# Kernel tuning notes

Hardware: AMD Instinct MI355X
Metric: run time of the kernel (lower is better)

The kernel has to match this reference:

```python
import jax, jax.numpy as jnp
import numpy as np

B, S, D = 4, 4096, 64

def setup_inputs() -> dict:
    key = jax.random.key(0)
    ks = jax.random.split(key, 6)
    mk = lambda k: jax.random.normal(k, (B, S, D), dtype=jnp.float32)
    return {
        "q_re": mk(ks[0]), "q_im": mk(ks[1]),
        "k_re": mk(ks[2]), "k_im": mk(ks[3]),
        "v_re": mk(ks[4]), "v_im": mk(ks[5]),
    }

def reference(q_re, q_im, k_re, k_im, v_re, v_im):
    # Complex QK^T (no conjugate, matching torch.bmm on complex tensors):
    # (qr + i qi)(kr + i ki)^T -> re = qr kr^T - qi ki^T ; im = qr ki^T + qi kr^T
    d_k = q_re.shape[-1]
    scale = 1.0 / jnp.sqrt(jnp.asarray(d_k, dtype=q_re.dtype))
    s_re = (jnp.einsum('bqd,bkd->bqk', q_re, k_re)
            - jnp.einsum('bqd,bkd->bqk', q_im, k_im)) * scale
    s_im = (jnp.einsum('bqd,bkd->bqk', q_re, k_im)
            + jnp.einsum('bqd,bkd->bqk', q_im, k_re)) * scale
    # softmax over |scores| along key axis; weights are real (imag part is 0)
    w = jax.nn.softmax(jnp.sqrt(s_re * s_re + s_im * s_im), axis=-1)  # [B,S,S]
    # CVDropout is identity in eval mode. Output = real_weights @ complex_values
    o_re = jnp.einsum('bqk,bkd->bqd', w, v_re)
    o_im = jnp.einsum('bqk,bkd->bqd', w, v_im)
    return jnp.stack([o_re, o_im], axis=0)  # [2, B, S, D] (real, imag)
```

## Files before the change

### kernel.cpp

```cpp
#include <hip/hip_runtime.h>
#include <stdint.h>

#define B_    4
#define S_    4096
#define D_    64
#define QBLK  64
#define NELEM (B_ * S_ * D_)
#define BS_   (B_ * S_)

typedef __attribute__((ext_vector_type(8))) short bf16x8;
typedef __attribute__((ext_vector_type(4))) short bf16x4;
typedef __attribute__((ext_vector_type(4))) float f32x4;
typedef __attribute__((ext_vector_type(4))) int   i32x4;
typedef __attribute__((ext_vector_type(4))) unsigned u32x4;
typedef __attribute__((ext_vector_type(4))) _Float16 f16x4;

#define MFMA(a, b, c) __builtin_amdgcn_mfma_f32_16x16x32_bf16(a, b, c, 0, 0, 0)
#define VMWAIT(n) asm volatile("s_waitcnt vmcnt(" #n ")" ::: "memory")
#define BARRIER() do { asm volatile("" ::: "memory"); __builtin_amdgcn_s_barrier(); asm volatile("" ::: "memory"); } while (0)
#define LGKM_FENCE() do { asm volatile("s_waitcnt lgkmcnt(0)" ::: "memory"); __builtin_amdgcn_sched_barrier(0); } while (0)

__device__ __forceinline__ short f2bf(float x) {
    unsigned u = __builtin_bit_cast(unsigned, x);
    u += 0x7FFFu + ((u >> 16) & 1u);
    return (short)(u >> 16);
}

__device__ __forceinline__ unsigned cvtpk(float lo, float hi) {
    unsigned r;
    asm("v_cvt_pk_bf16_f32 %0, %1, %2" : "=v"(r) : "v"(lo), "v"(hi));
    return r;
}

__device__ __forceinline__ void async16(const short* g, short* l) {
    __builtin_amdgcn_global_load_lds(
        (const __attribute__((address_space(1))) unsigned int*)g,
        (__attribute__((address_space(3))) unsigned int*)l, 16, 0, 0);
}

__global__ __launch_bounds__(256)
void prepass_kernel(const float* __restrict__ q_re, const float* __restrict__ q_im,
                    const float* __restrict__ k_re, const float* __restrict__ k_im,
                    const float* __restrict__ v_re, const float* __restrict__ v_im,
                    short* __restrict__ ws) {
    const int bidx = blockIdx.x;
    const int tid  = threadIdx.x;
    if (bidx < 4096) {
        const int idx = bidx * 256 + tid;
        const int tn  = idx >> 18;
        const int e4  = idx & ((1 << 18) - 1);
        const float* s = (tn == 0 ? q_re : tn == 1 ? q_im : tn == 2 ? k_re : k_im)
                         + (size_t)e4 * 4;
        const float sc = (tn < 2) ? 0.125f : 1.0f;
        f32x4 x = *(const f32x4*)s;
        bf16x4 v;
#pragma unroll
        for (int c = 0; c < 4; ++c) v[c] = f2bf(x[c] * sc);
        *(bf16x4*)(ws + (size_t)tn * NELEM + (size_t)e4 * 4) = v;
    } else {
        __shared__ short tile[64][72];
        const int tb   = bidx - 4096;
        const int sb   = tb & 63;
        const int b    = (tb >> 6) & 3;
        const int comp = tb >> 8;
        const float* src = comp ? v_im : v_re;
        short* dst = ws + (size_t)(4 + comp) * NELEM;
#pragma unroll
        for (int i = 0; i < 4; ++i) {
            const int slot = i * 256 + tid;
            const int s  = slot >> 4;
            const int d4 = slot & 15;
            f32x4 x = *(const f32x4*)(src + (((size_t)b * S_) + sb * 64 + s) * D_ + d4 * 4);
#pragma unroll
            for (int c = 0; c < 4; ++c) tile[d4 * 4 + c][s] = f2bf(x[c]);
        }
        __syncthreads();
#pragma unroll
        for (int i = 0; i < 2; ++i) {
            const int slot = i * 256 + tid;
            const int d = slot >> 3;
            const int m = slot & 7;
            const int a = m >> 2, hh = m & 3;
            bf16x8 v;
#pragma unroll
            for (int j = 0; j < 8; ++j)
                v[j] = tile[d][a * 32 + hh * 4 + ((j >> 2) << 4) + (j & 3)];
            *(bf16x8*)(dst + ((size_t)b * 64 + d) * S_ + sb * 64 + m * 8) = v;
        }
    }
}

template<int SPLIT, typename OT>
__global__ __launch_bounds__(256, 4)
void cv_attn_main(const short* __restrict__ wsb,
                  float* __restrict__ out,
                  OT* __restrict__ opart,
                  float* __restrict__ ml)
{
    __shared__ __align__(16) short smem[2 * 8192];

    const int tid  = threadIdx.x;
    const int lane = tid & 63;
    const int wv   = tid >> 6;
    const int l15  = lane & 15;
    const int h    = lane >> 4;

    int bid = blockIdx.x;
    const int nwg = B_ * 64 * SPLIT;
    bid = (bid & 7) * (nwg >> 3) + (bid >> 3);
    const int qb = bid & 63;
    const int sp = (bid >> 6) % SPLIT;
    const int b  = bid / (64 * SPLIT);

    const short* qr = wsb;
    const short* qi = wsb + (size_t)NELEM;
    const short* kr = wsb + 2 * (size_t)NELEM;
    const short* ki = wsb + 3 * (size_t)NELEM;
    const short* vT = wsb + 4 * (size_t)NELEM;

    const short* p0 = smem + l15 * 64 + ((h ^ (l15 & 7)) << 3);
    const short* p1 = smem + l15 * 64 + (((h ^ 4) ^ (l15 & 7)) << 3);

    const int qrow = qb * QBLK + wv * 16 + l15;
    const size_t qoff = ((size_t)b * S_ + qrow) * D_;
    bf16x8 fqr[2], fqi[2];
#pragma unroll
    for (int dh = 0; dh < 2; ++dh) {
        fqr[dh] = *(const bf16x8*)(qr + qoff + dh * 32 + h * 8);
        fqi[dh] = *(const bf16x8*)(qi + qoff + dh * 32 + h * 8);
    }

    f32x4 o_re[4], o_im[4];
#pragma unroll
    for (int i = 0; i < 4; ++i) {
        o_re[i] = (f32x4){0.f, 0.f, 0.f, 0.f};
        o_im[i] = (f32x4){0.f, 0.f, 0.f, 0.f};
    }
    float m_run = -1e30f, l_run = 0.f;
    const float L2E = 1.44269504088896f;

    const int srcg = (lane & 7) ^ (lane >> 3);
    const int kRow = wv * 8 + (lane >> 3);
    constexpr int TPB = (S_ / 32) / SPLIT;

    auto stageK = [&](int t, int DST) {
        const int kb = (sp * TPB + t) * 32;
        const size_t koff = ((size_t)b * S_ + kb + kRow) * 64 + (srcg << 3);
        async16(kr + koff, smem + DST + wv * 512);
        async16(ki + koff, smem + DST + 2048 + wv * 512);
    };
    auto stageV = [&](int t, int DST) {
        const int kb = (sp * TPB + t) * 32;
#pragma unroll
        for (int i = 0; i < 2; ++i) {
            const int d = (wv + 4 * i) * 8 + (lane >> 3);
            const short* src = vT + ((srcg >> 2) ? (size_t)NELEM : (size_t)0)
                               + ((size_t)b * 64 + d) * S_ + kb + (srcg & 3) * 8;
            async16(src, smem + DST + 4096 + wv * 512 + i * 2048);
        }
    };

    auto qk = [&](int CUR, f32x4 (&sre)[2], f32x4 (&sim)[2]) {
#pragma unroll
        for (int c = 0; c < 2; ++c) {
            sre[c] = (f32x4){0.f, 0.f, 0.f, 0.f};
            sim[c] = (f32x4){0.f, 0.f, 0.f, 0.f};
        }
        i32x4 n0 = __builtin_bit_cast(i32x4, fqi[0]) ^ (int)0x80008000;
        i32x4 n1 = __builtin_bit_cast(i32x4, fqi[1]) ^ (int)0x80008000;
        bf16x8 fn0 = __builtin_bit_cast(bf16x8, n0);
        bf16x8 fn1 = __builtin_bit_cast(bf16x8, n1);
        __builtin_amdgcn_s_setprio(1);
#pragma unroll
        for (int c = 0; c < 2; ++c) {
            bf16x8 a0 = *(const bf16x8*)(p0 + CUR + c * 1024);
            bf16x8 a1 = *(const bf16x8*)(p1 + CUR + c * 1024);
            bf16x8 b0 = *(const bf16x8*)(p0 + CUR + 2048 + c * 1024);
            bf16x8 b1 = *(const bf16x8*)(p1 + CUR + 2048 + c * 1024);
            sre[c] = MFMA(a0, fqr[0], sre[c]);
            sre[c] = MFMA(a1, fqr[1], sre[c]);
            sre[c] = MFMA(b0, fn0,    sre[c]);
            sre[c] = MFMA(b1, fn1,    sre[c]);
            sim[c] = MFMA(b0, fqr[0], sim[c]);
            sim[c] = MFMA(b1, fqr[1], sim[c]);
            sim[c] = MFMA(a0, fqi[0], sim[c]);
            sim[c] = MFMA(a1, fqi[1], sim[c]);
        }
        __builtin_amdgcn_s_setprio(0);
    };

    auto spv = [&](int CUR, f32x4 (&sre)[2], f32x4 (&sim)[2]) {
#pragma unroll
        for (int c = 0; c < 2; ++c) {
            f32x4 g = sre[c] * sre[c] + sim[c] * sim[c];
#pragma unroll
            for (int r = 0; r < 4; ++r) sre[c][r] = __builtin_amdgcn_sqrtf(g[r]);
        }
        float tmax = fmaxf(fmaxf(fmaxf(sre[0][0], sre[0][1]), fmaxf(sre[0][2], sre[0][3])),
                           fmaxf(fmaxf(sre[1][0], sre[1][1]), fmaxf(sre[1][2], sre[1][3])));
        tmax = fmaxf(tmax, __shfl_xor(tmax, 16));
        tmax = fmaxf(tmax, __shfl_xor(tmax, 32));
        if (__any(tmax > m_run + 8.0f)) {
            const float m_new = fmaxf(m_run, tmax);
            const float alpha = __builtin_amdgcn_exp2f((m_run - m_new) * L2E);
            l_run *= alpha;
#pragma unroll
            for (int i = 0; i < 4; ++i) { o_re[i] *= alpha; o_im[i] *= alpha; }
            m_run = m_new;
        }
        const float nm = -m_run * L2E;
#pragma unroll
        for (int c = 0; c < 2; ++c)
#pragma unroll
            for (int r = 0; r < 4; ++r)
                sim[c][r] = __builtin_amdgcn_exp2f(__builtin_fmaf(sre[c][r], L2E, nm));
        f32x4 ps = sim[0] + sim[1];
        l_run += (ps[0] + ps[1]) + (ps[2] + ps[3]);

        u32x4 w;
        w[0] = cvtpk(sim[0][0], sim[0][1]);
        w[1] = cvtpk(sim[0][2], sim[0][3]);
        w[2] = cvtpk(sim[1][0], sim[1][1]);
        w[3] = cvtpk(sim[1][2], sim[1][3]);
        bf16x8 pb = __builtin_bit_cast(bf16x8, w);

        __builtin_amdgcn_s_setprio(1);
#pragma unroll
        for (int dc = 0; dc < 4; ++dc) {
            bf16x8 av = *(const bf16x8*)(p0 + CUR + 4096 + dc * 1024);
            bf16x8 ai = *(const bf16x8*)(p1 + CUR + 4096 + dc * 1024);
            o_re[dc] = MFMA(av, pb, o_re[dc]);
            o_im[dc] = MFMA(ai, pb, o_im[dc]);
        }
        __builtin_amdgcn_s_setprio(0);
    };

    auto body = [&](int t, int CUR, int NXT,
                    f32x4 (&cre)[2], f32x4 (&cim)[2],
                    f32x4 (&nre)[2], f32x4 (&nim)[2]) {
        VMWAIT(0);
        LGKM_FENCE();
        BARRIER();
        if (t + 2 < TPB) stageK(t + 2, CUR);
        if (t + 1 < TPB) {
            stageV(t + 1, NXT);
            qk(NXT, nre, nim);
        }
        spv(CUR, cre, cim);
    };

    f32x4 sAre[2], sAim[2], sBre[2], sBim[2];
    stageK(0, 0);
    stageV(0, 0);
    stageK(1, 8192);
    VMWAIT(0);
    BARRIER();
    qk(0, sAre, sAim);

    for (int t = 0; t < TPB; t += 2) {
        body(t,     0,    8192, sAre, sAim, sBre, sBim);
        body(t + 1, 8192, 0,    sBre, sBim, sAre, sAim);
    }

    float lt = l_run;
    lt += __shfl_xor(lt, 16);
    lt += __shfl_xor(lt, 32);
    const float inv = 1.0f / lt;

    float* ol = (float*)smem;

    OT* dst_re;
    OT* dst_im;
    if constexpr (SPLIT == 1) {
        dst_re = (OT*)out + ((size_t)b * S_ + qb * QBLK) * D_;
        dst_im = dst_re + (size_t)NELEM;
    } else {
        const size_t qo = ((size_t)b * S_ + qb * QBLK) * D_;
        dst_re = opart + ((size_t)sp * 2 + 0) * NELEM + qo;
        dst_im = opart + ((size_t)sp * 2 + 1) * NELEM + qo;
    }

    auto store_comp = [&](const f32x4 (&oc)[4], OT* og) {
        __syncthreads();
#pragma unroll
        for (int dc = 0; dc < 4; ++dc)
#pragma unroll
            for (int r = 0; r < 4; ++r)
                ol[(wv * 16 + l15) * 65 + dc * 16 + h * 4 + r] = oc[dc][r] * inv;
        __syncthreads();
#pragma unroll
        for (int i = 0; i < 4; ++i) {
            const int slot = i * 256 + tid;
            const int row  = slot >> 4;
            const int c4   = slot & 15;
            f32x4 v;
#pragma unroll
            for (int j = 0; j < 4; ++j) v[j] = ol[row * 65 + c4 * 4 + j];
            if constexpr (sizeof(OT) == 4) {
                *(f32x4*)((float*)og + (size_t)row * D_ + c4 * 4) = v;
            } else {
                f16x4 hv;
#pragma unroll
                for (int j = 0; j < 4; ++j) hv[j] = (_Float16)v[j];
                *(f16x4*)((_Float16*)og + (size_t)row * D_ + c4 * 4) = hv;
            }
        }
    };
    store_comp(o_re, dst_re);
    store_comp(o_im, dst_im);

    if constexpr (SPLIT > 1) {
        if (lane < 16) {
            const int row = qb * QBLK + wv * 16 + lane;
            const size_t mo = ((size_t)sp * BS_ + (size_t)b * S_ + row) * 2;
            ml[mo]     = m_run;
            ml[mo + 1] = lt;
        }
    }
}

template<int SPLIT, typename OT>
__global__ __launch_bounds__(256)
void cv_attn_combine(const OT* __restrict__ opart, const float* __restrict__ ml,
                     float* __restrict__ out) {
    const int idx  = blockIdx.x * 256 + threadIdx.x;
    const int d4   = idx & 15;
    const int rest = idx >> 4;
    const int row  = rest & (BS_ - 1);
    const int comp = rest >> 14;
    float ms[SPLIT], ls[SPLIT];
    float M = -1e30f;
#pragma unroll
    for (int s = 0; s < SPLIT; ++s) {
        ms[s] = ml[((size_t)s * BS_ + row) * 2];
        ls[s] = ml[((size_t)s * BS_ + row) * 2 + 1];
        M = fmaxf(M, ms[s]);
    }
    float W = 0.f;
    f32x4 acc = (f32x4){0.f, 0.f, 0.f, 0.f};
#pragma unroll
    for (int s = 0; s < SPLIT; ++s) {
        const float w = ls[s] * __builtin_amdgcn_exp2f((ms[s] - M) * 1.44269504088896f);
        W += w;
        const OT* op = opart + ((size_t)(s * 2 + comp)) * NELEM + (size_t)row * D_ + d4 * 4;
        f32x4 o;
        if constexpr (sizeof(OT) == 4) {
            o = *(const f32x4*)op;
        } else {
            f16x4 hv = *(const f16x4*)op;
#pragma unroll
            for (int j = 0; j < 4; ++j) o[j] = (float)hv[j];
        }
        acc += o * w;
    }
    acc *= (1.0f / W);
    *(f32x4*)(out + (size_t)comp * NELEM + (size_t)row * D_ + d4 * 4) = acc;
}

__global__ __launch_bounds__(256, 1)
void cv_attn_legacy(const float* __restrict__ q_re, const float* __restrict__ q_im,
                    const float* __restrict__ k_re, const float* __restrict__ k_im,
                    const float* __restrict__ v_re, const float* __restrict__ v_im,
                    float* __restrict__ out)
{
    __shared__ __align__(16) short smem[4 * 64 * D_];
    short* kr_s = smem;
    short* ki_s = smem + 4096;
    short* vr_s = smem + 8192;
    short* vi_s = smem + 12288;

    const int tid  = threadIdx.x;
    const int lane = tid & 63;
    const int wv   = tid >> 6;
    const int l15  = lane & 15;
    const int h    = lane >> 4;

    const int b  = blockIdx.x >> 6;
    const int qb = blockIdx.x & 63;
    const size_t boff = (size_t)b * S_ * D_;

    const int qrow = qb * QBLK + wv * 16 + l15;
    const float* qrp = q_re + boff + (size_t)qrow * D_;
    const float* qip = q_im + boff + (size_t)qrow * D_;
    bf16x8 fqr[2], fqi[2], fqn[2];
#pragma unroll
    for (int dh = 0; dh < 2; ++dh) {
        const int d0 = dh * 32 + h * 8;
        f32x4 a0 = *(const f32x4*)(qrp + d0);
        f32x4 a1 = *(const f32x4*)(qrp + d0 + 4);
        f32x4 b0 = *(const f32x4*)(qip + d0);
        f32x4 b1 = *(const f32x4*)(qip + d0 + 4);
#pragma unroll
        for (int j = 0; j < 4; ++j) {
            fqr[dh][j] = f2bf(a0[j]); fqr[dh][j + 4] = f2bf(a1[j]);
            fqi[dh][j] = f2bf(b0[j]); fqi[dh][j + 4] = f2bf(b1[j]);
            fqn[dh][j] = f2bf(-b0[j]); fqn[dh][j + 4] = f2bf(-b1[j]);
        }
    }

    f32x4 o_re[4], o_im[4];
#pragma unroll
    for (int i = 0; i < 4; ++i) {
        o_re[i] = (f32x4){0.f, 0.f, 0.f, 0.f};
        o_im[i] = (f32x4){0.f, 0.f, 0.f, 0.f};
    }
    float m_run = -1e30f, l_run = 0.f;
    const float SC = 0.125f * 1.44269504088896f;

    for (int t = 0; t < S_ / 64; ++t) {
        const int kb = t * 64;
#pragma unroll
        for (int a = 0; a < 2; ++a) {
            const float* src = (a ? k_im : k_re) + boff;
            short* dst = a ? ki_s : kr_s;
#pragma unroll
            for (int i = 0; i < 2; ++i) {
                const int slot = i * 256 + tid;
                const int row  = slot >> 3;
                const int cb   = slot & 7;
                const float* p = src + (size_t)(kb + row) * D_ + cb * 8;
                f32x4 x0 = *(const f32x4*)p;
                f32x4 x1 = *(const f32x4*)(p + 4);
                bf16x8 v;
#pragma unroll
                for (int j = 0; j < 4; ++j) { v[j] = f2bf(x0[j]); v[j + 4] = f2bf(x1[j]); }
                *(bf16x8*)(dst + row * 64 + ((cb ^ (row & 7)) << 3)) = v;
            }
        }
#pragma unroll
        for (int a = 0; a < 2; ++a) {
            const float* src = (a ? v_im : v_re) + boff;
            short* dst = a ? vi_s : vr_s;
#pragma unroll
            for (int i = 0; i < 4; ++i) {
                const int slot = i * 256 + tid;
                const int k  = slot >> 4;
                const int d4 = slot & 15;
                f32x4 x = *(const f32x4*)(src + (size_t)(kb + k) * D_ + d4 * 4);
#pragma unroll
                for (int c = 0; c < 4; ++c) {
                    const int d = d4 * 4 + c;
                    dst[d * 64 + (((k >> 2) ^ (d & 15)) << 2) + (k & 3)] = f2bf(x[c]);
                }
            }
        }
        __syncthreads();

        f32x4 s_re[4], s_im[4];
#pragma unroll
        for (int c = 0; c < 4; ++c) {
            s_re[c] = (f32x4){0.f, 0.f, 0.f, 0.f};
            s_im[c] = (f32x4){0.f, 0.f, 0.f, 0.f};
        }
#pragma unroll
        for (int c = 0; c < 4; ++c) {
            const int krow = c * 16 + l15;
#pragma unroll
            for (int dh = 0; dh < 2; ++dh) {
                const int u = ((dh * 4 + h) ^ (krow & 7)) << 3;
                bf16x8 fkr = *(const bf16x8*)(kr_s + krow * 64 + u);
                bf16x8 fki = *(const bf16x8*)(ki_s + krow * 64 + u);
                s_re[c] = MFMA(fkr, fqr[dh], s_re[c]);
                s_re[c] = MFMA(fki, fqn[dh], s_re[c]);
                s_im[c] = MFMA(fki, fqr[dh], s_im[c]);
                s_im[c] = MFMA(fkr, fqi[dh], s_im[c]);
            }
        }

        float pv[4][4];
        float tmax = 0.f;
#pragma unroll
        for (int c = 0; c < 4; ++c)
#pragma unroll
            for (int r = 0; r < 4; ++r) {
                const float re = s_re[c][r], im = s_im[c][r];
                const float mg = __builtin_amdgcn_sqrtf(re * re + im * im) * SC;
                pv[c][r] = mg;
                tmax = fmaxf(tmax, mg);
            }
        tmax = fmaxf(tmax, __shfl_xor(tmax, 16));
        tmax = fmaxf(tmax, __shfl_xor(tmax, 32));
        const float m_new = fmaxf(m_run, tmax);
        const float alpha = __builtin_amdgcn_exp2f(m_run - m_new);
        m_run = m_new;
        float psum = 0.f;
#pragma unroll
        for (int c = 0; c < 4; ++c)
#pragma unroll
            for (int r = 0; r < 4; ++r) {
                const float e = __builtin_amdgcn_exp2f(pv[c][r] - m_new);
                pv[c][r] = e;
                psum += e;
            }
        l_run = l_run * alpha + psum;
#pragma unroll
        for (int i = 0; i < 4; ++i) { o_re[i] *= alpha; o_im[i] *= alpha; }

        bf16x8 pb[2];
#pragma unroll
        for (int hf = 0; hf < 2; ++hf)
#pragma unroll
            for (int j = 0; j < 4; ++j) {
                pb[hf][j]     = f2bf(pv[hf * 2][j]);
                pb[hf][j + 4] = f2bf(pv[hf * 2 + 1][j]);
            }

#pragma unroll
        for (int hf = 0; hf < 2; ++hf) {
#pragma unroll
            for (int dc = 0; dc < 4; ++dc) {
                const int d  = dc * 16 + l15;
                const int s0 = (((hf * 8) + h)     ^ l15) << 2;
                const int s1 = (((hf * 8) + 4 + h) ^ l15) << 2;
                bf16x4 r0 = *(const bf16x4*)(vr_s + d * 64 + s0);
                bf16x4 r1 = *(const bf16x4*)(vr_s + d * 64 + s1);
                bf16x4 i0 = *(const bf16x4*)(vi_s + d * 64 + s0);
                bf16x4 i1 = *(const bf16x4*)(vi_s + d * 64 + s1);
                bf16x8 av, ai;
#pragma unroll
                for (int j = 0; j < 4; ++j) {
                    av[j] = r0[j]; av[j + 4] = r1[j];
                    ai[j] = i0[j]; ai[j + 4] = i1[j];
                }
                o_re[dc] = MFMA(av, pb[hf], o_re[dc]);
                o_im[dc] = MFMA(ai, pb[hf], o_im[dc]);
            }
        }
        __syncthreads();
    }

    float lt = l_run;
    lt += __shfl_xor(lt, 16);
    lt += __shfl_xor(lt, 32);
    const float inv = 1.0f / lt;

    float* ol = (float*)smem;
    auto store_comp = [&](const f32x4 (&oc)[4], float* og) {
#pragma unroll
        for (int dc = 0; dc < 4; ++dc)
#pragma unroll
            for (int r = 0; r < 4; ++r)
                ol[(wv * 16 + l15) * 65 + dc * 16 + h * 4 + r] = oc[dc][r] * inv;
        __syncthreads();
#pragma unroll
        for (int i = 0; i < 4; ++i) {
            const int slot = i * 256 + tid;
            const int row  = slot >> 4;
            const int c4   = slot & 15;
            f32x4 v;
#pragma unroll
            for (int j = 0; j < 4; ++j) v[j] = ol[row * 65 + c4 * 4 + j];
            *(f32x4*)(og + (size_t)row * D_ + c4 * 4) = v;
        }
        __syncthreads();
    };

    float* og0 = out + boff + (size_t)(qb * QBLK) * D_;
    store_comp(o_re, og0);
    store_comp(o_im, og0 + (size_t)B_ * S_ * D_);
}

extern "C" void kernel_launch(void* const* d_in, const int* in_sizes, int n_in,
                              void* d_out, int out_size, void* d_ws, size_t ws_size,
                              hipStream_t stream) {
    (void)in_sizes; (void)n_in; (void)out_size;
    const float* q_re = (const float*)d_in[0];
    const float* q_im = (const float*)d_in[1];
    const float* k_re = (const float*)d_in[2];
    const float* k_im = (const float*)d_in[3];
    const float* v_re = (const float*)d_in[4];
    const float* v_im = (const float*)d_in[5];
    float* out = (float*)d_out;

    const size_t bf_bytes = 6 * (size_t)NELEM * 2;
    const size_t need8f16 = bf_bytes + 8 * 2 * (size_t)NELEM * 2 + 8 * (size_t)BS_ * 8;
    const size_t need4f16 = bf_bytes + 4 * 2 * (size_t)NELEM * 2 + 4 * (size_t)BS_ * 8;

    if (ws_size >= bf_bytes) {
        short* wsb = (short*)d_ws;
        prepass_kernel<<<4608, 256, 0, stream>>>(q_re, q_im, k_re, k_im, v_re, v_im, wsb);
        char* extra = (char*)d_ws + bf_bytes;
        if (ws_size >= need8f16) {
            _Float16* opart = (_Float16*)extra;
            float* ml = (float*)(extra + 8 * 2 * (size_t)NELEM * 2);
            cv_attn_main<8, _Float16><<<B_ * 64 * 8, 256, 0, stream>>>(wsb, nullptr, opart, ml);
            cv_attn_combine<8, _Float16><<<2048, 256, 0, stream>>>(opart, ml, out);
        } else if (ws_size >= need4f16) {
            _Float16* opart = (_Float16*)extra;
            float* ml = (float*)(extra + 4 * 2 * (size_t)NELEM * 2);
            cv_attn_main<4, _Float16><<<B_ * 64 * 4, 256, 0, stream>>>(wsb, nullptr, opart, ml);
            cv_attn_combine<4, _Float16><<<2048, 256, 0, stream>>>(opart, ml, out);
        } else {
            cv_attn_main<1, float><<<B_ * 64, 256, 0, stream>>>(wsb, out, out, nullptr);
        }
    } else {
        cv_attn_legacy<<<B_ * 64, 256, 0, stream>>>(q_re, q_im, k_re, k_im, v_re, v_im, out);
    }
}
```

Measured before the change: 91.45 us.

## Double query block per workgroup to 128 rows with 512 threads, simplify pipeline

The main attention kernel now processes 128 query rows per workgroup with 8 waves, so each staged K/V tile in shared memory is reused by twice as many waves, which halves the global-to-LDS traffic per query. The previous software pipeline, which overlapped the QK product of the next tile with the softmax-PV of the current one, is replaced by a simpler double-buffered loop that stages the next tile and then runs QK and PV on the current tile. The output store is split into two halves to fit the existing LDS scratch. Dropping the QK lookahead may expose more latency per wave, and the larger blocks cut the number of workgroups in half.

Measured after the change: 81.40 us. 11.0% less time.

```diff
diff --git a/kernel.cpp b/kernel.cpp
--- a/kernel.cpp
+++ b/kernel.cpp
@@ -4,7 +4,7 @@
 #define B_    4
 #define S_    4096
 #define D_    64
-#define QBLK  64
+#define QBLK  128
 #define NELEM (B_ * S_ * D_)
 #define BS_   (B_ * S_)
 
@@ -91,7 +91,7 @@
 }
 
 template<int SPLIT, typename OT>
-__global__ __launch_bounds__(256, 4)
+__global__ __launch_bounds__(512, 4)
 void cv_attn_main(const short* __restrict__ wsb,
                   float* __restrict__ out,
                   OT* __restrict__ opart,
@@ -106,11 +106,11 @@
     const int h    = lane >> 4;
 
     int bid = blockIdx.x;
-    const int nwg = B_ * 64 * SPLIT;
+    const int nwg = B_ * 32 * SPLIT;
     bid = (bid & 7) * (nwg >> 3) + (bid >> 3);
-    const int qb = bid & 63;
-    const int sp = (bid >> 6) % SPLIT;
-    const int b  = bid / (64 * SPLIT);
+    const int qb = bid & 31;
+    const int sp = (bid >> 5) % SPLIT;
+    const int b  = bid / (32 * SPLIT);
 
     const short* qr = wsb;
     const short* qi = wsb + (size_t)NELEM;
@@ -140,31 +140,37 @@
     const float L2E = 1.44269504088896f;
 
     const int srcg = (lane & 7) ^ (lane >> 3);
-    const int kRow = wv * 8 + (lane >> 3);
     constexpr int TPB = (S_ / 32) / SPLIT;
 
-    auto stageK = [&](int t, int DST) {
+    auto stage = [&](int t, int DST) {
         const int kb = (sp * TPB + t) * 32;
-        const size_t koff = ((size_t)b * S_ + kb + kRow) * 64 + (srcg << 3);
-        async16(kr + koff, smem + DST + wv * 512);
-        async16(ki + koff, smem + DST + 2048 + wv * 512);
-    };
-    auto stageV = [&](int t, int DST) {
-        const int kb = (sp * TPB + t) * 32;
-#pragma unroll
-        for (int i = 0; i < 2; ++i) {
-            const int d = (wv + 4 * i) * 8 + (lane >> 3);
+        {
+            const int arr = wv >> 2;
+            const int w4  = wv & 3;
+            const int row = w4 * 8 + (lane >> 3);
+            const short* src = (arr ? ki : kr)
+                               + ((size_t)b * S_ + kb + row) * 64 + (srcg << 3);
+            async16(src, smem + DST + arr * 2048 + w4 * 512);
+        }
+        {
+            const int d = wv * 8 + (lane >> 3);
             const short* src = vT + ((srcg >> 2) ? (size_t)NELEM : (size_t)0)
                                + ((size_t)b * 64 + d) * S_ + kb + (srcg & 3) * 8;
-            async16(src, smem + DST + 4096 + wv * 512 + i * 2048);
+            async16(src, smem + DST + 4096 + wv * 512);
         }
     };
 
-    auto qk = [&](int CUR, f32x4 (&sre)[2], f32x4 (&sim)[2]) {
+    auto body = [&](int t, int CUR, int OTH) {
+        VMWAIT(0);
+        LGKM_FENCE();
+        BARRIER();
+        if (t + 1 < TPB) stage(t + 1, OTH);
+
+        f32x4 s_re[2], s_im[2];
 #pragma unroll
         for (int c = 0; c < 2; ++c) {
-            sre[c] = (f32x4){0.f, 0.f, 0.f, 0.f};
-            sim[c] = (f32x4){0.f, 0.f, 0.f, 0.f};
+            s_re[c] = (f32x4){0.f, 0.f, 0.f, 0.f};
+            s_im[c] = (f32x4){0.f, 0.f, 0.f, 0.f};
         }
         i32x4 n0 = __builtin_bit_cast(i32x4, fqi[0]) ^ (int)0x80008000;
         i32x4 n1 = __builtin_bit_cast(i32x4, fqi[1]) ^ (int)0x80008000;
@@ -177,29 +183,28 @@
             bf16x8 a1 = *(const bf16x8*)(p1 + CUR + c * 1024);
             bf16x8 b0 = *(const bf16x8*)(p0 + CUR + 2048 + c * 1024);
             bf16x8 b1 = *(const bf16x8*)(p1 + CUR + 2048 + c * 1024);
-            sre[c] = MFMA(a0, fqr[0], sre[c]);
-            sre[c] = MFMA(a1, fqr[1], sre[c]);
-            sre[c] = MFMA(b0, fn0,    sre[c]);
-            sre[c] = MFMA(b1, fn1,    sre[c]);
-            sim[c] = MFMA(b0, fqr[0], sim[c]);
-            sim[c] = MFMA(b1, fqr[1], sim[c]);
-            sim[c] = MFMA(a0, fqi[0], sim[c]);
-            sim[c] = MFMA(a1, fqi[1], sim[c]);
+            s_re[c] = MFMA(a0, fqr[0], s_re[c]);
+            s_re[c] = MFMA(a1, fqr[1], s_re[c]);
+            s_re[c] = MFMA(b0, fn0,    s_re[c]);
+            s_re[c] = MFMA(b1, fn1,    s_re[c]);
+            s_im[c] = MFMA(b0, fqr[0], s_im[c]);
+            s_im[c] = MFMA(b1, fqr[1], s_im[c]);
+            s_im[c] = MFMA(a0, fqi[0], s_im[c]);
+            s_im[c] = MFMA(a1, fqi[1], s_im[c]);
         }
         __builtin_amdgcn_s_setprio(0);
-    };
-
-    auto spv = [&](int CUR, f32x4 (&sre)[2], f32x4 (&sim)[2]) {
+
 #pragma unroll
         for (int c = 0; c < 2; ++c) {
-            f32x4 g = sre[c] * sre[c] + sim[c] * sim[c];
-#pragma unroll
-            for (int r = 0; r < 4; ++r) sre[c][r] = __builtin_amdgcn_sqrtf(g[r]);
-        }
-        float tmax = fmaxf(fmaxf(fmaxf(sre[0][0], sre[0][1]), fmaxf(sre[0][2], sre[0][3])),
-                           fmaxf(fmaxf(sre[1][0], sre[1][1]), fmaxf(sre[1][2], sre[1][3])));
+            f32x4 g = s_re[c] * s_re[c] + s_im[c] * s_im[c];
+#pragma unroll
+            for (int r = 0; r < 4; ++r) s_re[c][r] = __builtin_amdgcn_sqrtf(g[r]);
+        }
+        float tmax = fmaxf(fmaxf(fmaxf(s_re[0][0], s_re[0][1]), fmaxf(s_re[0][2], s_re[0][3])),
+                           fmaxf(fmaxf(s_re[1][0], s_re[1][1]), fmaxf(s_re[1][2], s_re[1][3])));
         tmax = fmaxf(tmax, __shfl_xor(tmax, 16));
         tmax = fmaxf(tmax, __shfl_xor(tmax, 32));
+
         if (__any(tmax > m_run + 8.0f)) {
             const float m_new = fmaxf(m_run, tmax);
             const float alpha = __builtin_amdgcn_exp2f((m_run - m_new) * L2E);
@@ -209,19 +214,20 @@
             m_run = m_new;
         }
         const float nm = -m_run * L2E;
+
 #pragma unroll
         for (int c = 0; c < 2; ++c)
 #pragma unroll
             for (int r = 0; r < 4; ++r)
-                sim[c][r] = __builtin_amdgcn_exp2f(__builtin_fmaf(sre[c][r], L2E, nm));
-        f32x4 ps = sim[0] + sim[1];
+                s_im[c][r] = __builtin_amdgcn_exp2f(__builtin_fmaf(s_re[c][r], L2E, nm));
+        f32x4 ps = s_im[0] + s_im[1];
         l_run += (ps[0] + ps[1]) + (ps[2] + ps[3]);
 
         u32x4 w;
-        w[0] = cvtpk(sim[0][0], sim[0][1]);
-        w[1] = cvtpk(sim[0][2], sim[0][3]);
-        w[2] = cvtpk(sim[1][0], sim[1][1]);
-        w[3] = cvtpk(sim[1][2], sim[1][3]);
+        w[0] = cvtpk(s_im[0][0], s_im[0][1]);
+        w[1] = cvtpk(s_im[0][2], s_im[0][3]);
+        w[2] = cvtpk(s_im[1][0], s_im[1][1]);
+        w[3] = cvtpk(s_im[1][2], s_im[1][3]);
         bf16x8 pb = __builtin_bit_cast(bf16x8, w);
 
         __builtin_amdgcn_s_setprio(1);
@@ -235,31 +241,10 @@
         __builtin_amdgcn_s_setprio(0);
     };
 
-    auto body = [&](int t, int CUR, int NXT,
-                    f32x4 (&cre)[2], f32x4 (&cim)[2],
-                    f32x4 (&nre)[2], f32x4 (&nim)[2]) {
-        VMWAIT(0);
-        LGKM_FENCE();
-        BARRIER();
-        if (t + 2 < TPB) stageK(t + 2, CUR);
-        if (t + 1 < TPB) {
-            stageV(t + 1, NXT);
-            qk(NXT, nre, nim);
-        }
-        spv(CUR, cre, cim);
-    };
-
-    f32x4 sAre[2], sAim[2], sBre[2], sBim[2];
-    stageK(0, 0);
-    stageV(0, 0);
-    stageK(1, 8192);
-    VMWAIT(0);
-    BARRIER();
-    qk(0, sAre, sAim);
-
-    for (int t = 0; t < TPB; t += 2) {
-        body(t,     0,    8192, sAre, sAim, sBre, sBim);
-        body(t + 1, 8192, 0,    sBre, sBim, sAre, sAim);
+    stage(0, 0);
+    for (int tt = 0; tt < TPB; tt += 2) {
+        body(tt,     0,    8192);
+        body(tt + 1, 8192, 0);
     }
 
     float lt = l_run;
@@ -281,28 +266,34 @@
     }
 
     auto store_comp = [&](const f32x4 (&oc)[4], OT* og) {
-        __syncthreads();
-#pragma unroll
-        for (int dc = 0; dc < 4; ++dc)
-#pragma unroll
-            for (int r = 0; r < 4; ++r)
-                ol[(wv * 16 + l15) * 65 + dc * 16 + h * 4 + r] = oc[dc][r] * inv;
-        __syncthreads();
-#pragma unroll
-        for (int i = 0; i < 4; ++i) {
-            const int slot = i * 256 + tid;
-            const int row  = slot >> 4;
-            const int c4   = slot & 15;
-            f32x4 v;
-#pragma unroll
-            for (int j = 0; j < 4; ++j) v[j] = ol[row * 65 + c4 * 4 + j];
-            if constexpr (sizeof(OT) == 4) {
-                *(f32x4*)((float*)og + (size_t)row * D_ + c4 * 4) = v;
-            } else {
-                f16x4 hv;
-#pragma unroll
-                for (int j = 0; j < 4; ++j) hv[j] = (_Float16)v[j];
-                *(f16x4*)((_Float16*)og + (size_t)row * D_ + c4 * 4) = hv;
+#pragma unroll
+        for (int half = 0; half < 2; ++half) {
+            __syncthreads();
+            if ((wv >> 2) == half) {
+                const int wl = wv & 3;
+#pragma unroll
+                for (int dc = 0; dc < 4; ++dc)
+#pragma unroll
+                    for (int r = 0; r < 4; ++r)
+                        ol[(wl * 16 + l15) * 65 + dc * 16 + h * 4 + r] = oc[dc][r] * inv;
+            }
+            __syncthreads();
+#pragma unroll
+            for (int i = 0; i < 2; ++i) {
+                const int slot = i * 512 + tid;
+                const int row  = slot >> 4;
+                const int c4   = slot & 15;
+                f32x4 v;
+#pragma unroll
+                for (int j = 0; j < 4; ++j) v[j] = ol[row * 65 + c4 * 4 + j];
+                if constexpr (sizeof(OT) == 4) {
+                    *(f32x4*)((float*)og + (size_t)(half * 64 + row) * D_ + c4 * 4) = v;
+                } else {
+                    f16x4 hv;
+#pragma unroll
+                    for (int j = 0; j < 4; ++j) hv[j] = (_Float16)v[j];
+                    *(f16x4*)((_Float16*)og + (size_t)(half * 64 + row) * D_ + c4 * 4) = hv;
+                }
             }
         }
     };
@@ -379,7 +370,7 @@
     const int qb = blockIdx.x & 63;
     const size_t boff = (size_t)b * S_ * D_;
 
-    const int qrow = qb * QBLK + wv * 16 + l15;
+    const int qrow = qb * 64 + wv * 16 + l15;
     const float* qrp = q_re + boff + (size_t)qrow * D_;
     const float* qip = q_im + boff + (size_t)qrow * D_;
     bf16x8 fqr[2], fqi[2], fqn[2];
@@ -555,7 +546,7 @@
         __syncthreads();
     };
 
-    float* og0 = out + boff + (size_t)(qb * QBLK) * D_;
+    float* og0 = out + boff + (size_t)(qb * 64) * D_;
     store_comp(o_re, og0);
     store_comp(o_im, og0 + (size_t)B_ * S_ * D_);
 }
@@ -583,15 +574,15 @@
         if (ws_size >= need8f16) {
             _Float16* opart = (_Float16*)extra;
             float* ml = (float*)(extra + 8 * 2 * (size_t)NELEM * 2);
-            cv_attn_main<8, _Float16><<<B_ * 64 * 8, 256, 0, stream>>>(wsb, nullptr, opart, ml);
+            cv_attn_main<8, _Float16><<<B_ * 32 * 8, 512, 0, stream>>>(wsb, nullptr, opart, ml);
             cv_attn_combine<8, _Float16><<<2048, 256, 0, stream>>>(opart, ml, out);
         } else if (ws_size >= need4f16) {
             _Float16* opart = (_Float16*)extra;
             float* ml = (float*)(extra + 4 * 2 * (size_t)NELEM * 2);
-            cv_attn_main<4, _Float16><<<B_ * 64 * 4, 256, 0, stream>>>(wsb, nullptr, opart, ml);
+            cv_attn_main<4, _Float16><<<B_ * 32 * 4, 512, 0, stream>>>(wsb, nullptr, opart, ml);
             cv_attn_combine<4, _Float16><<<2048, 256, 0, stream>>>(opart, ml, out);
         } else {
-            cv_attn_main<1, float><<<B_ * 64, 256, 0, stream>>>(wsb, out, out, nullptr);
+            cv_attn_main<1, float><<<B_ * 32, 512, 0, stream>>>(wsb, out, out, nullptr);
         }
     } else {
         cv_attn_legacy<<<B_ * 64, 256, 0, stream>>>(q_re, q_im, k_re, k_im, v_re, v_im, out);
```
